# Kernel tuning notes

Measured on AMD Instinct MI355X. Metric: run time of the kernel, lower is better.

Reference implementation:

```python
import jax, jax.numpy as jnp
import numpy as np

MASK_RADIUS = 30.0

def _fft_mask(height, width, mode):
    # replicates fft_filter_def: grid over full H rows and rfft half-plane cols
    cht, cwt = height // 2, width // 2
    fy, fx = jnp.meshgrid(jnp.arange(height), jnp.arange(width // 2 + 1), indexing='ij')
    dist = jnp.sqrt((fx - cwt).astype(jnp.float32) ** 2 + (fy - cht).astype(jnp.float32) ** 2)
    if mode == 'high':
        return (dist > MASK_RADIUS).astype(jnp.float32)
    return (dist <= MASK_RADIUS).astype(jnp.float32)


def setup_inputs() -> dict:
    key = jax.random.key(0)
    k1, k2, k3 = jax.random.split(key, 3)
    B, Cin, Cout, H, W, K = 4, 64, 64, 128, 128, 3
    x = jax.random.normal(k1, (B, Cin, H, W), dtype=jnp.float32)
    weight = jax.random.normal(k2, (Cout, Cin, K, K), dtype=jnp.float32) * 0.1
    bias = jax.random.normal(k3, (Cout,), dtype=jnp.float32) * 0.1
    return {"x": x, "weight": weight, "bias": bias}


def reference(x, weight, bias):
    B, Cin, H, W = x.shape
    x = x.astype(jnp.float32)
    # rfft2 of input, then fftshift (as in original; kernel FFT is NOT shifted)
    fft_x = jnp.fft.rfft2(x)                          # [B, Cin, H, W//2+1]
    fft_x = jnp.fft.fftshift(fft_x, axes=(-2, -1))
    kernel_fft = jnp.fft.rfft2(weight, s=(H, W))      # [Cout, Cin, H, W//2+1]
    # high-pass frequency mask (fft_filter == 'high')
    mask = _fft_mask(H, W, 'high')                    # [H, W//2+1]
    fft_x = fft_x * mask
    # per-frequency complex GEMV over in_channels (avoids [B,Cout,Cin,H,Wf] blowup)
    fft_out = jnp.einsum('bihw,oihw->bohw', fft_x, kernel_fft)
    out = jnp.fft.irfft2(fft_out, s=(H, W))           # [B, Cout, H, W]
    return out + bias[None, :, None, None]
```

## Files before the change

### kernel.cpp

```cpp
#include <hip/hip_runtime.h>

#define PI_F 3.14159265358979323846f

#define HH 128
#define WW 128
#define WF 65
#define NB 4
#define NC 64
#define CPLX_PER_IMG (HH * WF)

typedef __attribute__((ext_vector_type(8))) short short8;
typedef __attribute__((ext_vector_type(4))) float f32x4;

__device__ __forceinline__ ushort f2b(float f) {
    unsigned u = __float_as_uint(f);
    u += 0x7fffu + ((u >> 16) & 1u);
    return (ushort)(u >> 16);
}


__global__ __launch_bounds__(256) void k_pre(const float* __restrict__ w,
                                             ushort* __restrict__ A1,
                                             ushort* __restrict__ A2,
                                             ushort* __restrict__ A4,
                                             ushort* __restrict__ A5,
                                             ushort* __restrict__ WvRe,
                                             ushort* __restrict__ WvIm) {
    int idx = blockIdx.x * 256 + threadIdx.x;
    if (idx < 20480) {
        int m = idx >> 7, k = idx & 127;
        int part = m / 80, v = m - part * 80;
        float s, c;
        __sincosf(2.f * PI_F * (float)((v * k) & 127) / 128.f, &s, &c);
        float val = (v < 65) ? (part ? -s : c) : 0.f;
        A1[idx] = f2b(val);
    } else if (idx < 86016) {
        int j = idx - 20480;
        int m = j >> 8, k2 = j & 255;
        int part = m >> 7, u = m & 127;
        int kp = k2 >> 7, h = k2 & 127;
        float s, c;
        __sincosf(2.f * PI_F * (float)((u * h) & 127) / 128.f, &s, &c);
        float val = part == 0 ? (kp == 0 ? c : s) : (kp == 0 ? -s : c);
        A2[j] = f2b(val);
    } else if (idx < 151552) {
        int j = idx - 86016;
        int m = j >> 8, k2 = j & 255;
        int part = m >> 7, h = m & 127;
        int kp = k2 >> 7, u = k2 & 127;
        float s, c;
        __sincosf(2.f * PI_F * (float)((u * h) & 127) / 128.f, &s, &c);
        float val = part == 0 ? (kp == 0 ? c : -s) : (kp == 0 ? s : c);
        A4[j] = f2b(val * (1.f / 128.f));
    } else if (idx < 172032) {
        int j = idx - 151552;
        int x = j / 160, k2 = j - x * 160;
        int part = k2 / 80, v = k2 - part * 80;
        float s, c;
        __sincosf(2.f * PI_F * (float)((v * x) & 127) / 128.f, &s, &c);
        float cv = (v == 0 || v == 64) ? 1.f : 2.f;
        float val = (v < 65) ? (part == 0 ? cv * c : -cv * s) * (1.f / 128.f) : 0.f;
        A5[j] = f2b(val);
    } else {
        int xw = idx - 172032;
        int i = xw & 63;
        int o = (xw >> 6) & 63;
        int pv = xw >> 12;
        int p = pv / WF;
        int v = pv % WF;
        const float* wp = w + ((size_t)o * 64 + i) * 9 + p * 3;
        float re = wp[0], im = 0.f;
#pragma unroll
        for (int q = 1; q <= 2; ++q) {
            int k = (v * q) & 127;
            float s, c;
            __sincosf(-2.f * PI_F * (float)k / 128.f, &s, &c);
            re += wp[q] * c;
            im += wp[q] * s;
        }
        WvRe[xw] = f2b(re);
        WvIm[xw] = f2b(im);
    }
}

#define B1P 136
#define B2P 280
__global__ __launch_bounds__(1024) void k_fwd(const float* __restrict__ x,
                                              const ushort* __restrict__ A1,
                                              const ushort* __restrict__ A2,
                                              ushort* __restrict__ XsRe,
                                              ushort* __restrict__ XsIm) {
    __shared__ ushort B1[128 * B1P];
    __shared__ ushort B2[80 * B2P];
    int t = threadIdx.x;
    int img = blockIdx.x;
    const float* gx = x + (size_t)img * 16384;
    for (int c = t; c < 2048; c += 1024) {
        int r = c >> 4, sl = c & 15;
        const float* src = gx + r * 128 + sl * 8;
        float4 f0 = *(const float4*)src;
        float4 f1 = *(const float4*)(src + 4);
        short8 v8;
        v8[0] = (short)f2b(f0.x); v8[1] = (short)f2b(f0.y);
        v8[2] = (short)f2b(f0.z); v8[3] = (short)f2b(f0.w);
        v8[4] = (short)f2b(f1.x); v8[5] = (short)f2b(f1.y);
        v8[6] = (short)f2b(f1.z); v8[7] = (short)f2b(f1.w);
        *(short8*)&B1[r * B1P + sl * 8] = v8;
    }
    __syncthreads();
    int lane = t & 63, wave = t >> 6;
    int lrow = lane & 15, lq = lane >> 4;

    {
        int g = wave >> 3, nt = wave & 7;
        int hrow = nt * 16 + lrow;
        f32x4 acc[5];
#pragma unroll
        for (int j = 0; j < 5; ++j) acc[j] = (f32x4){0.f, 0.f, 0.f, 0.f};
#pragma unroll
        for (int ks = 0; ks < 4; ++ks) {
            short8 b = *(short8*)&B1[hrow * B1P + ks * 32 + lq * 8];
#pragma unroll
            for (int j = 0; j < 5; ++j) {
                int mt = g * 5 + j;
                short8 a = *(const short8*)&A1[(mt * 16 + lrow) * 128 + ks * 32 + lq * 8];
                acc[j] = __builtin_amdgcn_mfma_f32_16x16x32_bf16(a, b, acc[j], 0, 0, 0);
            }
        }
#pragma unroll
        for (int j = 0; j < 5; ++j) {
            int m0 = (g * 5 + j) * 16 + lq * 4;
            int part = m0 >= 80;
            int v0 = m0 - part * 80;
#pragma unroll
            for (int e = 0; e < 4; ++e)
                B2[(v0 + e) * B2P + part * 128 + hrow] = f2b(acc[j][e]);
        }
    }
    __syncthreads();

    {
        int nt = wave;
        f32x4 acc[5];
#pragma unroll
        for (int mt = 0; mt < 5; ++mt) acc[mt] = (f32x4){0.f, 0.f, 0.f, 0.f};
#pragma unroll
        for (int ks = 0; ks < 8; ++ks) {
            short8 b = *(const short8*)&A2[(nt * 16 + lrow) * 256 + ks * 32 + lq * 8];
#pragma unroll
            for (int mt = 0; mt < 5; ++mt) {
                short8 a = *(short8*)&B2[(mt * 16 + lrow) * B2P + ks * 32 + lq * 8];
                acc[mt] = __builtin_amdgcn_mfma_f32_16x16x32_bf16(a, b, acc[mt], 0, 0, 0);
            }
        }
        int part = nt >= 8;
        int u = (nt & 7) * 16 + lrow;
        int u_out = (u + 64) & 127;
        int du = u_out - 64;
        ushort* dimg = (part ? XsIm : XsRe) + (size_t)img * CPLX_PER_IMG;
#pragma unroll
        for (int mt = 0; mt < 5; ++mt)
#pragma unroll
            for (int e = 0; e < 4; ++e) {
                int v_in = mt * 16 + lq * 4 + e;
                if (v_in < 65) {
                    int v_out = v_in + 32; if (v_out >= 65) v_out -= 65;
                    int dv = v_out - 64;
                    bool keep = (du * du + dv * dv) > 900;
                    dimg[v_out * 128 + u_out] = keep ? f2b(acc[mt][e]) : (ushort)0;
                }
            }
    }
}

#define AP 72
__global__ __launch_bounds__(256, 2) void k_gemm(const ushort* __restrict__ XsRe,
                                                 const ushort* __restrict__ XsIm,
                                                 const ushort* __restrict__ WvRe,
                                                 const ushort* __restrict__ WvIm,
                                                 ushort* __restrict__ Zre,
                                                 ushort* __restrict__ Zim) {
    __shared__ ushort XTre[128 * AP], XTim[128 * AP];
    __shared__ ushort WSre[64 * AP],  WSim[64 * AP];
    int t = threadIdx.x;
    int v = blockIdx.x >> 2;
    int b = blockIdx.x & 3;
    {
        int u = t & 127, qh = t >> 7;
#pragma unroll
        for (int q8 = 0; q8 < 8; ++q8) {
            int q = qh * 8 + q8;
            ushort re4[4], im4[4];
#pragma unroll
            for (int c = 0; c < 4; ++c) {
                int i = q * 4 + c;
                size_t off = ((size_t)(b * 64 + i) * WF + v) * 128 + u;
                re4[c] = XsRe[off];
                im4[c] = XsIm[off];
            }
            *(ushort4*)&XTre[u * AP + q * 4] = make_ushort4(re4[0], re4[1], re4[2], re4[3]);
            *(ushort4*)&XTim[u * AP + q * 4] = make_ushort4(im4[0], im4[1], im4[2], im4[3]);
        }
    }
    int lane = t & 63, wave = t >> 6;
    int lrow = lane & 15, lq = lane >> 4;
    int u0 = wave * 32;
    f32x4 fRe[8], fIm[8];
#pragma unroll
    for (int m = 0; m < 8; ++m) {
        fRe[m] = (f32x4){0.f, 0.f, 0.f, 0.f};
        fIm[m] = (f32x4){0.f, 0.f, 0.f, 0.f};
    }
    for (int p = 0; p < 3; ++p) {
        if (p) __syncthreads();
        {
            const ushort* gr = WvRe + ((size_t)(p * WF + v)) * 4096;
            const ushort* gi = WvIm + ((size_t)(p * WF + v)) * 4096;
#pragma unroll
            for (int cc = 0; cc < 2; ++cc) {
                int c = t + cc * 256;
                int o = c >> 3, i0 = (c & 7) * 8;
                *(short8*)&WSre[o * AP + i0] = *(const short8*)&gr[c * 8];
                *(short8*)&WSim[o * AP + i0] = *(const short8*)&gi[c * 8];
            }
        }
        __syncthreads();
        f32x4 pRe[8], pIm[8];
#pragma unroll
        for (int m = 0; m < 8; ++m) {
            pRe[m] = (f32x4){0.f, 0.f, 0.f, 0.f};
            pIm[m] = (f32x4){0.f, 0.f, 0.f, 0.f};
        }
#pragma unroll
        for (int ks = 0; ks < 2; ++ks) {
            int kb = ks * 32 + lq * 8;
            short8 br[2], bi[2], bin[2];
#pragma unroll
            for (int ut = 0; ut < 2; ++ut) {
                int u = u0 + ut * 16 + lrow;
                br[ut] = *(const short8*)&XTre[u * AP + kb];
                bi[ut] = *(const short8*)&XTim[u * AP + kb];
                bin[ut] = bi[ut] ^ (short)0x8000;
            }
#pragma unroll
            for (int ot = 0; ot < 4; ++ot) {
                int o = ot * 16 + lrow;
                short8 ar = *(const short8*)&WSre[o * AP + kb];
                short8 ai = *(const short8*)&WSim[o * AP + kb];
#pragma unroll
                for (int ut = 0; ut < 2; ++ut) {
                    int m = ot * 2 + ut;
                    pRe[m] = __builtin_amdgcn_mfma_f32_16x16x32_bf16(ai, bin[ut], pRe[m], 0, 0, 0);
                    pRe[m] = __builtin_amdgcn_mfma_f32_16x16x32_bf16(ar, br[ut],  pRe[m], 0, 0, 0);
                    pIm[m] = __builtin_amdgcn_mfma_f32_16x16x32_bf16(ai, br[ut],  pIm[m], 0, 0, 0);
                    pIm[m] = __builtin_amdgcn_mfma_f32_16x16x32_bf16(ar, bi[ut],  pIm[m], 0, 0, 0);
                }
            }
        }
#pragma unroll
        for (int ut = 0; ut < 2; ++ut) {
            int u = u0 + ut * 16 + lrow;
            float sn, cn;
            __sincosf(-2.f * PI_F * (float)(u * p) / 128.f, &sn, &cn);
#pragma unroll
            for (int ot = 0; ot < 4; ++ot) {
                int m = ot * 2 + ut;
#pragma unroll
                for (int e = 0; e < 4; ++e) {
                    fRe[m][e] += pRe[m][e] * cn - pIm[m][e] * sn;
                    fIm[m][e] += pIm[m][e] * cn + pRe[m][e] * sn;
                }
            }
        }
    }
#pragma unroll
    for (int ot = 0; ot < 4; ++ot)
#pragma unroll
        for (int ut = 0; ut < 2; ++ut) {
            int m = ot * 2 + ut;
            int u = u0 + ut * 16 + lrow;
#pragma unroll
            for (int e = 0; e < 4; ++e) {
                int o = ot * 16 + lq * 4 + e;
                size_t idx = ((size_t)(b * 64 + o) * 65 + v) * 128 + u;
                Zre[idx] = f2b(fRe[m][e]);
                Zim[idx] = f2b(fIm[m][e]);
            }
        }
}

#define B3P 168
__global__ __launch_bounds__(1024) void k_inv(const ushort* __restrict__ Zre,
                                              const ushort* __restrict__ Zim,
                                              const ushort* __restrict__ A4,
                                              const ushort* __restrict__ A5,
                                              const float* __restrict__ bias,
                                              float* __restrict__ out) {
    __shared__ ushort B1[80 * B2P];
    __shared__ ushort B2[128 * B3P];
    int t = threadIdx.x;
    int ch = blockIdx.x;
    for (int c = t; c < 2080; c += 1024) {
        int r = c >> 5, sl = c & 31;
        const ushort* src = (sl < 16 ? Zre : Zim) + ((size_t)ch * 65 + r) * 128 + (sl & 15) * 8;
        *(short8*)&B1[r * B2P + sl * 8] = *(const short8*)src;
    }
    if (t < 480) {
        int r = 65 + (t >> 5), sl = t & 31;
        short8 z = {0, 0, 0, 0, 0, 0, 0, 0};
        *(short8*)&B1[r * B2P + sl * 8] = z;
    }
    __syncthreads();
    int lane = t & 63, wave = t >> 6;
    int lrow = lane & 15, lq = lane >> 4;

    {
        int mt = wave;
        f32x4 acc[5];
#pragma unroll
        for (int nt = 0; nt < 5; ++nt) acc[nt] = (f32x4){0.f, 0.f, 0.f, 0.f};
#pragma unroll
        for (int ks = 0; ks < 8; ++ks) {
            short8 a = *(const short8*)&A4[(mt * 16 + lrow) * 256 + ks * 32 + lq * 8];
#pragma unroll
            for (int nt = 0; nt < 5; ++nt) {
                short8 b = *(short8*)&B1[(nt * 16 + lrow) * B2P + ks * 32 + lq * 8];
                acc[nt] = __builtin_amdgcn_mfma_f32_16x16x32_bf16(a, b, acc[nt], 0, 0, 0);
            }
        }
        int part = mt >= 8;
        int h0 = mt * 16 + lq * 4 - part * 128;
#pragma unroll
        for (int nt = 0; nt < 5; ++nt) {
            int v = nt * 16 + lrow;
#pragma unroll
            for (int e = 0; e < 4; ++e)
                B2[(h0 + e) * B3P + part * 80 + v] = f2b(acc[nt][e]);
        }
    }
    __syncthreads();

    {
        int mt = wave & 7, nh = wave >> 3;
        f32x4 acc[4];
#pragma unroll
        for (int jn = 0; jn < 4; ++jn) acc[jn] = (f32x4){0.f, 0.f, 0.f, 0.f};
#pragma unroll
        for (int ks = 0; ks < 5; ++ks) {
            short8 a = *(short8*)&B2[(mt * 16 + lrow) * B3P + ks * 32 + lq * 8];
#pragma unroll
            for (int jn = 0; jn < 4; ++jn) {
                int nt = nh * 4 + jn;
                short8 b = *(const short8*)&A5[(nt * 16 + lrow) * 160 + ks * 32 + lq * 8];
                acc[jn] = __builtin_amdgcn_mfma_f32_16x16x32_bf16(a, b, acc[jn], 0, 0, 0);
            }
        }
        float bo = bias[ch & 63];
        float* go = out + (size_t)ch * 16384;
#pragma unroll
        for (int jn = 0; jn < 4; ++jn) {
            int xx = (nh * 4 + jn) * 16 + lrow;
#pragma unroll
            for (int e = 0; e < 4; ++e) {
                int h = mt * 16 + lq * 4 + e;
                go[h * 128 + xx] = acc[jn][e] + bo;
            }
        }
    }
}

extern "C" void kernel_launch(void* const* d_in, const int* in_sizes, int n_in,
                              void* d_out, int out_size, void* d_ws, size_t ws_size,
                              hipStream_t stream) {
    const float* x = (const float*)d_in[0];
    const float* w = (const float*)d_in[1];
    const float* bias = (const float*)d_in[2];
    float* out = (float*)d_out;

    char* ws = (char*)d_ws;
    ushort* A1   = (ushort*)(ws + 0);
    ushort* A2   = (ushort*)(ws + 40960);
    ushort* A4   = (ushort*)(ws + 172032);
    ushort* A5   = (ushort*)(ws + 303104);
    ushort* WvRe = (ushort*)(ws + 344064);
    ushort* WvIm = (ushort*)(ws + 1941504);
    ushort* XsRe = (ushort*)(ws + 12058624);
    ushort* XsIm = (ushort*)(ws + 16318464);
    ushort* Zre  = (ushort*)(ws + 20578304);
    ushort* Zim  = (ushort*)(ws + 24838144);

    k_pre<<<3792, 256, 0, stream>>>(w, A1, A2, A4, A5, WvRe, WvIm);
    k_fwd<<<NB * NC, 1024, 0, stream>>>(x, A1, A2, XsRe, XsIm);
    k_gemm<<<WF * NB, 256, 0, stream>>>(XsRe, XsIm, WvRe, WvIm, Zre, Zim);
    k_inv<<<NB * NC, 1024, 0, stream>>>(Zre, Zim, A4, A5, bias, out);
}
```

Baseline: 54.21 us.

## Split precompute: build DFT matrices first, compute weight spectra inside forward-FFT kernel

The precompute kernel now only produces the A1/A2 forward DFT matrices (the first 86016 items, 84 blocks of 1024). The remaining A4/A5 inverse matrices and the weight-spectrum items run in 54 extra blocks appended to the forward-transform launch, overlapping that work with the per-image forward FFT. This shortens the serialized precompute stage. In exchange, k_fwd gets more parameters and extra blocks that compete for CUs, and the coverage must exactly match the item count (54*16*1024 ≈ 884736 items beyond 86016).

```diff
diff --git a/kernel.cpp b/kernel.cpp
--- a/kernel.cpp
+++ b/kernel.cpp
@@ -19,14 +19,10 @@
 }
 
 
-__global__ __launch_bounds__(256) void k_pre(const float* __restrict__ w,
-                                             ushort* __restrict__ A1,
-                                             ushort* __restrict__ A2,
-                                             ushort* __restrict__ A4,
-                                             ushort* __restrict__ A5,
-                                             ushort* __restrict__ WvRe,
-                                             ushort* __restrict__ WvIm) {
-    int idx = blockIdx.x * 256 + threadIdx.x;
+__device__ __forceinline__ void pre_item(int idx, const float* __restrict__ w,
+                                         ushort* __restrict__ A1, ushort* __restrict__ A2,
+                                         ushort* __restrict__ A4, ushort* __restrict__ A5,
+                                         ushort* __restrict__ WvRe, ushort* __restrict__ WvIm) {
     if (idx < 20480) {
         int m = idx >> 7, k = idx & 127;
         int part = m / 80, v = m - part * 80;
@@ -83,17 +79,41 @@
     }
 }
 
+__global__ __launch_bounds__(1024) void k_preA(const float* __restrict__ w,
+                                               ushort* __restrict__ A1,
+                                               ushort* __restrict__ A2,
+                                               ushort* __restrict__ A4,
+                                               ushort* __restrict__ A5,
+                                               ushort* __restrict__ WvRe,
+                                               ushort* __restrict__ WvIm) {
+    int idx = blockIdx.x * 1024 + threadIdx.x;
+    pre_item(idx, w, A1, A2, A4, A5, WvRe, WvIm);
+}
+
 #define B1P 136
 #define B2P 280
 __global__ __launch_bounds__(1024) void k_fwd(const float* __restrict__ x,
+                                              const float* __restrict__ w,
                                               const ushort* __restrict__ A1,
                                               const ushort* __restrict__ A2,
+                                              ushort* __restrict__ A4,
+                                              ushort* __restrict__ A5,
+                                              ushort* __restrict__ WvRe,
+                                              ushort* __restrict__ WvIm,
                                               ushort* __restrict__ XsRe,
                                               ushort* __restrict__ XsIm) {
     __shared__ ushort B1[128 * B1P];
     __shared__ ushort B2[80 * B2P];
     int t = threadIdx.x;
-    int img = blockIdx.x;
+    int bid = blockIdx.x;
+    if (bid >= 256) {
+        int base = 86016 + ((bid - 256) * 16) * 1024 + t;
+#pragma unroll 2
+        for (int k = 0; k < 16; ++k)
+            pre_item(base + k * 1024, w, (ushort*)A1, (ushort*)A2, A4, A5, WvRe, WvIm);
+        return;
+    }
+    int img = bid;
     const float* gx = x + (size_t)img * 16384;
     for (int c = t; c < 2048; c += 1024) {
         int r = c >> 4, sl = c & 15;
@@ -282,7 +302,7 @@
 #pragma unroll
             for (int e = 0; e < 4; ++e) {
                 int o = ot * 16 + lq * 4 + e;
-                size_t idx = ((size_t)(b * 64 + o) * 65 + v) * 128 + u;
+                size_t idx = ((size_t)(b * 64 + o) * WF + v) * 128 + u;
                 Zre[idx] = f2b(fRe[m][e]);
                 Zim[idx] = f2b(fIm[m][e]);
             }
@@ -302,7 +322,7 @@
     int ch = blockIdx.x;
     for (int c = t; c < 2080; c += 1024) {
         int r = c >> 5, sl = c & 31;
-        const ushort* src = (sl < 16 ? Zre : Zim) + ((size_t)ch * 65 + r) * 128 + (sl & 15) * 8;
+        const ushort* src = (sl < 16 ? Zre : Zim) + ((size_t)ch * WF + r) * 128 + (sl & 15) * 8;
         *(short8*)&B1[r * B2P + sl * 8] = *(const short8*)src;
     }
     if (t < 480) {
@@ -389,8 +409,8 @@
     ushort* Zre  = (ushort*)(ws + 20578304);
     ushort* Zim  = (ushort*)(ws + 24838144);
 
-    k_pre<<<3792, 256, 0, stream>>>(w, A1, A2, A4, A5, WvRe, WvIm);
-    k_fwd<<<NB * NC, 1024, 0, stream>>>(x, A1, A2, XsRe, XsIm);
+    k_preA<<<84, 1024, 0, stream>>>(w, A1, A2, A4, A5, WvRe, WvIm);
+    k_fwd<<<256 + 54, 1024, 0, stream>>>(x, w, A1, A2, A4, A5, WvRe, WvIm, XsRe, XsIm);
     k_gemm<<<WF * NB, 256, 0, stream>>>(XsRe, XsIm, WvRe, WvIm, Zre, Zim);
     k_inv<<<NB * NC, 1024, 0, stream>>>(Zre, Zim, A4, A5, bias, out);
 }
```

After: 58.20 us. 1.07x slower.

## Fuse kernel-weight DFT into GEMM and move inverse-table setup into GEMM

Applied to the files above, without the earlier changes.

Removes the precomputed bf16 per-frequency weight spectra (WvRe/WvIm) and instead computes the 3-tap row DFT of the conv weights on the fly inside k_gemm from the raw fp32 weights, using per-block twiddles. The A4/A5 inverse DFT tables are now generated by the GEMM blocks, and the prepass kernel shrinks to only A1/A2. This drops a large workspace write/read of roughly 3 MB and most of the prepass work. In exchange each GEMM block does redundant strided fp32 weight loads and extra ALU work, with some risk of slower staging.

```diff
diff --git a/kernel.cpp b/kernel.cpp
--- a/kernel.cpp
+++ b/kernel.cpp
@@ -19,14 +19,9 @@
 }
 
 
-__global__ __launch_bounds__(256) void k_pre(const float* __restrict__ w,
-                                             ushort* __restrict__ A1,
-                                             ushort* __restrict__ A2,
-                                             ushort* __restrict__ A4,
-                                             ushort* __restrict__ A5,
-                                             ushort* __restrict__ WvRe,
-                                             ushort* __restrict__ WvIm) {
-    int idx = blockIdx.x * 256 + threadIdx.x;
+__device__ __forceinline__ void pre_item12(int idx,
+                                           ushort* __restrict__ A1,
+                                           ushort* __restrict__ A2) {
     if (idx < 20480) {
         int m = idx >> 7, k = idx & 127;
         int part = m / 80, v = m - part * 80;
@@ -34,7 +29,7 @@
         __sincosf(2.f * PI_F * (float)((v * k) & 127) / 128.f, &s, &c);
         float val = (v < 65) ? (part ? -s : c) : 0.f;
         A1[idx] = f2b(val);
-    } else if (idx < 86016) {
+    } else {
         int j = idx - 20480;
         int m = j >> 8, k2 = j & 255;
         int part = m >> 7, u = m & 127;
@@ -43,7 +38,13 @@
         __sincosf(2.f * PI_F * (float)((u * h) & 127) / 128.f, &s, &c);
         float val = part == 0 ? (kp == 0 ? c : s) : (kp == 0 ? -s : c);
         A2[j] = f2b(val);
-    } else if (idx < 151552) {
+    }
+}
+
+__device__ __forceinline__ void pre_item45(int idx,
+                                           ushort* __restrict__ A4,
+                                           ushort* __restrict__ A5) {
+    if (idx < 151552) {
         int j = idx - 86016;
         int m = j >> 8, k2 = j & 255;
         int part = m >> 7, h = m & 127;
@@ -52,7 +53,7 @@
         __sincosf(2.f * PI_F * (float)((u * h) & 127) / 128.f, &s, &c);
         float val = part == 0 ? (kp == 0 ? c : -s) : (kp == 0 ? s : c);
         A4[j] = f2b(val * (1.f / 128.f));
-    } else if (idx < 172032) {
+    } else {
         int j = idx - 151552;
         int x = j / 160, k2 = j - x * 160;
         int part = k2 / 80, v = k2 - part * 80;
@@ -61,26 +62,13 @@
         float cv = (v == 0 || v == 64) ? 1.f : 2.f;
         float val = (v < 65) ? (part == 0 ? cv * c : -cv * s) * (1.f / 128.f) : 0.f;
         A5[j] = f2b(val);
-    } else {
-        int xw = idx - 172032;
-        int i = xw & 63;
-        int o = (xw >> 6) & 63;
-        int pv = xw >> 12;
-        int p = pv / WF;
-        int v = pv % WF;
-        const float* wp = w + ((size_t)o * 64 + i) * 9 + p * 3;
-        float re = wp[0], im = 0.f;
-#pragma unroll
-        for (int q = 1; q <= 2; ++q) {
-            int k = (v * q) & 127;
-            float s, c;
-            __sincosf(-2.f * PI_F * (float)k / 128.f, &s, &c);
-            re += wp[q] * c;
-            im += wp[q] * s;
-        }
-        WvRe[xw] = f2b(re);
-        WvIm[xw] = f2b(im);
-    }
+    }
+}
+
+__global__ __launch_bounds__(256) void k_preA(ushort* __restrict__ A1,
+                                              ushort* __restrict__ A2) {
+    int idx = blockIdx.x * 256 + threadIdx.x;
+    pre_item12(idx, A1, A2);
 }
 
 #define B1P 136
@@ -176,8 +164,9 @@
 #define AP 72
 __global__ __launch_bounds__(256, 2) void k_gemm(const ushort* __restrict__ XsRe,
                                                  const ushort* __restrict__ XsIm,
-                                                 const ushort* __restrict__ WvRe,
-                                                 const ushort* __restrict__ WvIm,
+                                                 const float* __restrict__ w,
+                                                 ushort* __restrict__ A4,
+                                                 ushort* __restrict__ A5,
                                                  ushort* __restrict__ Zre,
                                                  ushort* __restrict__ Zim) {
     __shared__ ushort XTre[128 * AP], XTim[128 * AP];
@@ -185,6 +174,14 @@
     int t = threadIdx.x;
     int v = blockIdx.x >> 2;
     int b = blockIdx.x & 3;
+
+    {
+        int gtid = blockIdx.x * 256 + t;
+#pragma unroll 2
+        for (int idx = 86016 + gtid; idx < 172032; idx += 66560)
+            pre_item45(idx, A4, A5);
+    }
+
     {
         int u = t & 127, qh = t >> 7;
 #pragma unroll
@@ -202,6 +199,14 @@
             *(ushort4*)&XTim[u * AP + q * 4] = make_ushort4(im4[0], im4[1], im4[2], im4[3]);
         }
     }
+
+    float s1v, c1v, s2v, c2v;
+    {
+        int k1 = v & 127, k2 = (2 * v) & 127;
+        __sincosf(-2.f * PI_F * (float)k1 / 128.f, &s1v, &c1v);
+        __sincosf(-2.f * PI_F * (float)k2 / 128.f, &s2v, &c2v);
+    }
+
     int lane = t & 63, wave = t >> 6;
     int lrow = lane & 15, lq = lane >> 4;
     int u0 = wave * 32;
@@ -214,14 +219,24 @@
     for (int p = 0; p < 3; ++p) {
         if (p) __syncthreads();
         {
-            const ushort* gr = WvRe + ((size_t)(p * WF + v)) * 4096;
-            const ushort* gi = WvIm + ((size_t)(p * WF + v)) * 4096;
 #pragma unroll
             for (int cc = 0; cc < 2; ++cc) {
                 int c = t + cc * 256;
                 int o = c >> 3, i0 = (c & 7) * 8;
-                *(short8*)&WSre[o * AP + i0] = *(const short8*)&gr[c * 8];
-                *(short8*)&WSim[o * AP + i0] = *(const short8*)&gi[c * 8];
+                const float* wb = w + ((size_t)(o * 64 + i0)) * 9 + p * 3;
+                short8 vre, vim;
+#pragma unroll
+                for (int e = 0; e < 8; ++e) {
+                    float w0 = wb[e * 9 + 0];
+                    float w1 = wb[e * 9 + 1];
+                    float w2 = wb[e * 9 + 2];
+                    float re = w0 + w1 * c1v + w2 * c2v;
+                    float im = w1 * s1v + w2 * s2v;
+                    vre[e] = (short)f2b(re);
+                    vim[e] = (short)f2b(im);
+                }
+                *(short8*)&WSre[o * AP + i0] = vre;
+                *(short8*)&WSim[o * AP + i0] = vim;
             }
         }
         __syncthreads();
@@ -282,7 +297,7 @@
 #pragma unroll
             for (int e = 0; e < 4; ++e) {
                 int o = ot * 16 + lq * 4 + e;
-                size_t idx = ((size_t)(b * 64 + o) * 65 + v) * 128 + u;
+                size_t idx = ((size_t)(b * 64 + o) * WF + v) * 128 + u;
                 Zre[idx] = f2b(fRe[m][e]);
                 Zim[idx] = f2b(fIm[m][e]);
             }
@@ -302,7 +317,7 @@
     int ch = blockIdx.x;
     for (int c = t; c < 2080; c += 1024) {
         int r = c >> 5, sl = c & 31;
-        const ushort* src = (sl < 16 ? Zre : Zim) + ((size_t)ch * 65 + r) * 128 + (sl & 15) * 8;
+        const ushort* src = (sl < 16 ? Zre : Zim) + ((size_t)ch * WF + r) * 128 + (sl & 15) * 8;
         *(short8*)&B1[r * B2P + sl * 8] = *(const short8*)src;
     }
     if (t < 480) {
@@ -382,15 +397,13 @@
     ushort* A2   = (ushort*)(ws + 40960);
     ushort* A4   = (ushort*)(ws + 172032);
     ushort* A5   = (ushort*)(ws + 303104);
-    ushort* WvRe = (ushort*)(ws + 344064);
-    ushort* WvIm = (ushort*)(ws + 1941504);
     ushort* XsRe = (ushort*)(ws + 12058624);
     ushort* XsIm = (ushort*)(ws + 16318464);
     ushort* Zre  = (ushort*)(ws + 20578304);
     ushort* Zim  = (ushort*)(ws + 24838144);
 
-    k_pre<<<3792, 256, 0, stream>>>(w, A1, A2, A4, A5, WvRe, WvIm);
+    k_preA<<<336, 256, 0, stream>>>(A1, A2);
     k_fwd<<<NB * NC, 1024, 0, stream>>>(x, A1, A2, XsRe, XsIm);
-    k_gemm<<<WF * NB, 256, 0, stream>>>(XsRe, XsIm, WvRe, WvIm, Zre, Zim);
+    k_gemm<<<WF * NB, 256, 0, stream>>>(XsRe, XsIm, w, A4, A5, Zre, Zim);
     k_inv<<<NB * NC, 1024, 0, stream>>>(Zre, Zim, A4, A5, bias, out);
 }
```

Measured after the change: 58.43 us. +7.8%, slower.

## Split forward and inverse DFT blocks into two halves of 512 threads

Applied to the files above, without the earlier changes.

k_fwd and k_inv now launch 512 blocks of 512 threads instead of 256 blocks of 1024. Each forward block recomputes the full first-stage row transform and produces only half of the second-stage output columns. Each inverse block computes only the half of the rows it writes, which also halves the second shared buffer. The aim is to fill the GPU's 256 CUs better and lower per-block latency, at the cost of repeating the first-stage work and the input staging loads in both halves.

```diff
diff --git a/kernel.cpp b/kernel.cpp
--- a/kernel.cpp
+++ b/kernel.cpp
@@ -85,17 +85,18 @@
 
 #define B1P 136
 #define B2P 280
-__global__ __launch_bounds__(1024) void k_fwd(const float* __restrict__ x,
-                                              const ushort* __restrict__ A1,
-                                              const ushort* __restrict__ A2,
-                                              ushort* __restrict__ XsRe,
-                                              ushort* __restrict__ XsIm) {
+__global__ __launch_bounds__(512) void k_fwd(const float* __restrict__ x,
+                                             const ushort* __restrict__ A1,
+                                             const ushort* __restrict__ A2,
+                                             ushort* __restrict__ XsRe,
+                                             ushort* __restrict__ XsIm) {
     __shared__ ushort B1[128 * B1P];
     __shared__ ushort B2[80 * B2P];
     int t = threadIdx.x;
-    int img = blockIdx.x;
+    int img = blockIdx.x & 255;
+    int half = blockIdx.x >> 8;
     const float* gx = x + (size_t)img * 16384;
-    for (int c = t; c < 2048; c += 1024) {
+    for (int c = t; c < 2048; c += 512) {
         int r = c >> 4, sl = c & 15;
         const float* src = gx + r * 128 + sl * 8;
         float4 f0 = *(const float4*)src;
@@ -112,24 +113,22 @@
     int lrow = lane & 15, lq = lane >> 4;
 
     {
-        int g = wave >> 3, nt = wave & 7;
-        int hrow = nt * 16 + lrow;
-        f32x4 acc[5];
-#pragma unroll
-        for (int j = 0; j < 5; ++j) acc[j] = (f32x4){0.f, 0.f, 0.f, 0.f};
+        int hrow = wave * 16 + lrow;
+        f32x4 acc[10];
+#pragma unroll
+        for (int j = 0; j < 10; ++j) acc[j] = (f32x4){0.f, 0.f, 0.f, 0.f};
 #pragma unroll
         for (int ks = 0; ks < 4; ++ks) {
             short8 b = *(short8*)&B1[hrow * B1P + ks * 32 + lq * 8];
 #pragma unroll
-            for (int j = 0; j < 5; ++j) {
-                int mt = g * 5 + j;
-                short8 a = *(const short8*)&A1[(mt * 16 + lrow) * 128 + ks * 32 + lq * 8];
+            for (int j = 0; j < 10; ++j) {
+                short8 a = *(const short8*)&A1[(j * 16 + lrow) * 128 + ks * 32 + lq * 8];
                 acc[j] = __builtin_amdgcn_mfma_f32_16x16x32_bf16(a, b, acc[j], 0, 0, 0);
             }
         }
 #pragma unroll
-        for (int j = 0; j < 5; ++j) {
-            int m0 = (g * 5 + j) * 16 + lq * 4;
+        for (int j = 0; j < 10; ++j) {
+            int m0 = j * 16 + lq * 4;
             int part = m0 >= 80;
             int v0 = m0 - part * 80;
 #pragma unroll
@@ -140,7 +139,7 @@
     __syncthreads();
 
     {
-        int nt = wave;
+        int nt = half * 8 + wave;
         f32x4 acc[5];
 #pragma unroll
         for (int mt = 0; mt < 5; ++mt) acc[mt] = (f32x4){0.f, 0.f, 0.f, 0.f};
@@ -282,7 +281,7 @@
 #pragma unroll
             for (int e = 0; e < 4; ++e) {
                 int o = ot * 16 + lq * 4 + e;
-                size_t idx = ((size_t)(b * 64 + o) * 65 + v) * 128 + u;
+                size_t idx = ((size_t)(b * 64 + o) * WF + v) * 128 + u;
                 Zre[idx] = f2b(fRe[m][e]);
                 Zim[idx] = f2b(fIm[m][e]);
             }
@@ -290,19 +289,20 @@
 }
 
 #define B3P 168
-__global__ __launch_bounds__(1024) void k_inv(const ushort* __restrict__ Zre,
-                                              const ushort* __restrict__ Zim,
-                                              const ushort* __restrict__ A4,
-                                              const ushort* __restrict__ A5,
-                                              const float* __restrict__ bias,
-                                              float* __restrict__ out) {
+__global__ __launch_bounds__(512) void k_inv(const ushort* __restrict__ Zre,
+                                             const ushort* __restrict__ Zim,
+                                             const ushort* __restrict__ A4,
+                                             const ushort* __restrict__ A5,
+                                             const float* __restrict__ bias,
+                                             float* __restrict__ out) {
     __shared__ ushort B1[80 * B2P];
-    __shared__ ushort B2[128 * B3P];
+    __shared__ ushort B2[64 * B3P];
     int t = threadIdx.x;
-    int ch = blockIdx.x;
-    for (int c = t; c < 2080; c += 1024) {
+    int ch = blockIdx.x & 255;
+    int H = blockIdx.x >> 8;
+    for (int c = t; c < 2080; c += 512) {
         int r = c >> 5, sl = c & 31;
-        const ushort* src = (sl < 16 ? Zre : Zim) + ((size_t)ch * 65 + r) * 128 + (sl & 15) * 8;
+        const ushort* src = (sl < 16 ? Zre : Zim) + ((size_t)ch * WF + r) * 128 + (sl & 15) * 8;
         *(short8*)&B1[r * B2P + sl * 8] = *(const short8*)src;
     }
     if (t < 480) {
@@ -315,7 +315,8 @@
     int lrow = lane & 15, lq = lane >> 4;
 
     {
-        int mt = wave;
+        int part = wave >> 2, j = wave & 3;
+        int mt = part * 8 + H * 4 + j;
         f32x4 acc[5];
 #pragma unroll
         for (int nt = 0; nt < 5; ++nt) acc[nt] = (f32x4){0.f, 0.f, 0.f, 0.f};
@@ -328,26 +329,25 @@
                 acc[nt] = __builtin_amdgcn_mfma_f32_16x16x32_bf16(a, b, acc[nt], 0, 0, 0);
             }
         }
-        int part = mt >= 8;
-        int h0 = mt * 16 + lq * 4 - part * 128;
+        int h0l = j * 16 + lq * 4;
 #pragma unroll
         for (int nt = 0; nt < 5; ++nt) {
             int v = nt * 16 + lrow;
 #pragma unroll
             for (int e = 0; e < 4; ++e)
-                B2[(h0 + e) * B3P + part * 80 + v] = f2b(acc[nt][e]);
+                B2[(h0l + e) * B3P + part * 80 + v] = f2b(acc[nt][e]);
         }
     }
     __syncthreads();
 
     {
-        int mt = wave & 7, nh = wave >> 3;
+        int mtl = wave & 3, nh = wave >> 2;
         f32x4 acc[4];
 #pragma unroll
         for (int jn = 0; jn < 4; ++jn) acc[jn] = (f32x4){0.f, 0.f, 0.f, 0.f};
 #pragma unroll
         for (int ks = 0; ks < 5; ++ks) {
-            short8 a = *(short8*)&B2[(mt * 16 + lrow) * B3P + ks * 32 + lq * 8];
+            short8 a = *(short8*)&B2[(mtl * 16 + lrow) * B3P + ks * 32 + lq * 8];
 #pragma unroll
             for (int jn = 0; jn < 4; ++jn) {
                 int nt = nh * 4 + jn;
@@ -362,7 +362,7 @@
             int xx = (nh * 4 + jn) * 16 + lrow;
 #pragma unroll
             for (int e = 0; e < 4; ++e) {
-                int h = mt * 16 + lq * 4 + e;
+                int h = H * 64 + mtl * 16 + lq * 4 + e;
                 go[h * 128 + xx] = acc[jn][e] + bo;
             }
         }
@@ -390,7 +390,7 @@
     ushort* Zim  = (ushort*)(ws + 24838144);
 
     k_pre<<<3792, 256, 0, stream>>>(w, A1, A2, A4, A5, WvRe, WvIm);
-    k_fwd<<<NB * NC, 1024, 0, stream>>>(x, A1, A2, XsRe, XsIm);
+    k_fwd<<<512, 512, 0, stream>>>(x, A1, A2, XsRe, XsIm);
     k_gemm<<<WF * NB, 256, 0, stream>>>(XsRe, XsIm, WvRe, WvIm, Zre, Zim);
-    k_inv<<<NB * NC, 1024, 0, stream>>>(Zre, Zim, A4, A5, bias, out);
-}
+    k_inv<<<512, 512, 0, stream>>>(Zre, Zim, A4, A5, bias, out);
+}
```

Result: slower. 62.62 us (+15.5%).
